# Optimization experiments

Measured on AMD Instinct MI355X. Metric: run time of the kernel, lower is better.

Reference implementation:

```python
import jax, jax.numpy as jnp
import numpy as np


def setup_inputs() -> dict:
    key = jax.random.key(0)
    k1, k2, k3, k4, k5 = jax.random.split(key, 5)
    H = W = 128
    C = 256
    N = 2000
    A = 7
    features_map = jax.random.normal(k1, (1, H, W, C), dtype=jnp.float32)
    # valid integer boxes: x2 > x1, y2 > y1, in-bounds
    x1 = jax.random.randint(k2, (N,), 0, W - 8)
    y1 = jax.random.randint(k3, (N,), 0, H - 8)
    bw = jax.random.randint(k4, (N,), 4, 48)
    bh = jax.random.randint(k5, (N,), 4, 48)
    x2 = jnp.minimum(x1 + bw, W)
    y2 = jnp.minimum(y1 + bh, H)
    boxes = jnp.stack([x1, y1, x2, y2], axis=-1).astype(jnp.int32)
    return {"features_map": features_map, "boxes": boxes, "anchor_size": A}


def reference(features_map, boxes, anchor_size):
    # Fused ROI pooling: per box, bilinear-resize the crop [y1:y2, x1:x2]
    # to (anchor_size, anchor_size), matching tf.image.resize bilinear
    # (half-pixel centers, edge clamped inside the crop).
    A = int(anchor_size)
    fm = features_map[0]  # [H, W, C]

    def axis_samples(lo, hi):
        span = (hi - lo).astype(jnp.float32)
        src = (jnp.arange(A, dtype=jnp.float32) + 0.5) * (span / A) - 0.5
        src = jnp.clip(src, 0.0, jnp.maximum(span - 1.0, 0.0))
        i0 = jnp.floor(src).astype(jnp.int32)
        i1 = jnp.minimum(i0 + 1, hi - lo - 1)
        frac = src - i0.astype(jnp.float32)
        return i0 + lo, i1 + lo, frac

    def pool_one(box):
        x1, y1, x2, y2 = box[0], box[1], box[2], box[3]
        ys0, ys1, fy = axis_samples(y1, y2)  # [A]
        xs0, xs1, fx = axis_samples(x1, x2)  # [A]
        v00 = fm[ys0[:, None], xs0[None, :]]  # [A, A, C]
        v01 = fm[ys0[:, None], xs1[None, :]]
        v10 = fm[ys1[:, None], xs0[None, :]]
        v11 = fm[ys1[:, None], xs1[None, :]]
        fy_ = fy[:, None, None]
        fx_ = fx[None, :, None]
        top = v00 * (1.0 - fx_) + v01 * fx_
        bot = v10 * (1.0 - fx_) + v11 * fx_
        return (top * (1.0 - fy_) + bot * fy_)[None]  # [1, A, A, C]

    return jax.vmap(pool_one)(boxes)  # [N, 1, A, A, C]
```

## Files before the change

kernel.cpp:

```cpp
#include <hip/hip_runtime.h>
#include <hip/hip_bf16.h>
#include <hip/hip_fp16.h>


#define FM_H 128
#define FM_W 128
#define FM_C 256
#define ANCH 7
#define NSAMP (ANCH * ANCH)
#define FM_ELEMS (FM_H * FM_W * FM_C)
#define CONV_BLOCKS 256

typedef float   f4 __attribute__((ext_vector_type(4)));
typedef _Float16 h4 __attribute__((ext_vector_type(4)));

__global__ __launch_bounds__(256) void prep_kernel(
    const float* __restrict__ fm, const int* __restrict__ boxes,
    _Float16* __restrict__ fm16, int* __restrict__ order,
    int n_boxes, int conv_blocks)
{
    if ((int)blockIdx.x < conv_blocks) {
        const int tid = blockIdx.x * 256 + threadIdx.x;
        const f4* src = (const f4*)fm;
        h4* dst = (h4*)fm16;
        #pragma unroll
        for (int k = 0; k < 16; ++k) {
            const int i = tid + k * 65536;
            const f4 v = src[i];
            h4 h;
            h[0] = (_Float16)v[0]; h[1] = (_Float16)v[1];
            h[2] = (_Float16)v[2]; h[3] = (_Float16)v[3];
            dst[i] = h;
        }
        return;
    }

    __shared__ int cursor[64];
    const int tid = threadIdx.x;
    if (tid < 64) cursor[tid] = 0;
    __syncthreads();

    for (int i = tid; i < n_boxes; i += 256) {
        const int x1 = boxes[i * 4 + 0];
        const int y1 = boxes[i * 4 + 1];
        const int key = ((y1 >> 4) << 3) | (x1 >> 4);
        atomicAdd(&cursor[key], 1);
    }
    __syncthreads();

    if (tid == 0) {
        int run = 0;
        for (int k = 0; k < 64; ++k) { int c = cursor[k]; cursor[k] = run; run += c; }
    }
    __syncthreads();

    for (int i = tid; i < n_boxes; i += 256) {
        const int x1 = boxes[i * 4 + 0];
        const int y1 = boxes[i * 4 + 1];
        const int key = ((y1 >> 4) << 3) | (x1 >> 4);
        const int pos = atomicAdd(&cursor[key], 1);
        order[pos] = i;
    }
}

template <typename ET, typename V4>
__global__ __launch_bounds__(256) void roi_pool_kernel_t(
    const ET* __restrict__ fmx,
    const int* __restrict__ boxes,
    const int* __restrict__ order,
    float* __restrict__ out,
    int n_samples)
{
    const int nb  = gridDim.x;
    const int b   = blockIdx.x;
    const int q   = nb >> 3;
    const int r   = nb & 7;
    const int xcd = b & 7;
    const int idx = b >> 3;
    const int sb  = (xcd < r ? xcd * (q + 1) : r * (q + 1) + (xcd - r) * q) + idx;

    const int lane = threadIdx.x & 63;
    const int wave = __builtin_amdgcn_readfirstlane((sb << 2) + (threadIdx.x >> 6));
    if (wave >= n_samples) return;

    const int sorted_box = wave / NSAMP;
    const int s   = wave - sorted_box * NSAMP;
    const int py  = s / ANCH;
    const int px  = s - py * ANCH;
    const int box = order ? order[sorted_box] : sorted_box;

    const int x1 = boxes[box * 4 + 0];
    const int y1 = boxes[box * 4 + 1];
    const int x2 = boxes[box * 4 + 2];
    const int y2 = boxes[box * 4 + 3];

    const float spany = (float)(y2 - y1);
    float sy = ((float)py + 0.5f) * (spany / (float)ANCH) - 0.5f;
    sy = fminf(fmaxf(sy, 0.0f), fmaxf(spany - 1.0f, 0.0f));
    const int iy0 = (int)floorf(sy);
    const int iy1 = min(iy0 + 1, y2 - y1 - 1);
    const float fy = sy - (float)iy0;
    const int ys0 = iy0 + y1;
    const int ys1 = iy1 + y1;

    const float spanx = (float)(x2 - x1);
    float sx = ((float)px + 0.5f) * (spanx / (float)ANCH) - 0.5f;
    sx = fminf(fmaxf(sx, 0.0f), fmaxf(spanx - 1.0f, 0.0f));
    const int ix0 = (int)floorf(sx);
    const int ix1 = min(ix0 + 1, x2 - x1 - 1);
    const float fx = sx - (float)ix0;
    const int xs0 = ix0 + x1;
    const int xs1 = ix1 + x1;

    const V4* p00 = (const V4*)(fmx + ((size_t)(ys0 * FM_W + xs0)) * FM_C);
    const V4* p01 = (const V4*)(fmx + ((size_t)(ys0 * FM_W + xs1)) * FM_C);
    const V4* p10 = (const V4*)(fmx + ((size_t)(ys1 * FM_W + xs0)) * FM_C);
    const V4* p11 = (const V4*)(fmx + ((size_t)(ys1 * FM_W + xs1)) * FM_C);

    const V4 v00 = p00[lane];
    const V4 v01 = p01[lane];
    const V4 v10 = p10[lane];
    const V4 v11 = p11[lane];

    const float gx = 1.0f - fx;
    const float gy = 1.0f - fy;

    f4 res;
    #pragma unroll
    for (int c = 0; c < 4; ++c) {
        const float top = (float)v00[c] * gx + (float)v01[c] * fx;
        const float bot = (float)v10[c] * gx + (float)v11[c] * fx;
        res[c] = top * gy + bot * fy;
    }

    f4* dst = (f4*)(out + ((size_t)(box * NSAMP + s)) * FM_C);
    __builtin_nontemporal_store(res, &dst[lane]);
}

extern "C" void kernel_launch(void* const* d_in, const int* in_sizes, int n_in,
                              void* d_out, int out_size, void* d_ws, size_t ws_size,
                              hipStream_t stream) {
    const float* fm    = (const float*)d_in[0];
    const int*   boxes = (const int*)d_in[1];

    const int N = in_sizes[1] / 4;
    const int n_samples = N * NSAMP;
    float* out = (float*)d_out;

    const size_t f16_bytes   = (size_t)FM_ELEMS * sizeof(_Float16);
    const size_t order_bytes = (size_t)N * sizeof(int);

    const int threads = 256;
    const int grid = (n_samples + 3) / 4;

    if (ws_size >= f16_bytes + order_bytes) {
        _Float16* fm16 = (_Float16*)d_ws;
        int* order = (int*)((char*)d_ws + f16_bytes);

        prep_kernel<<<CONV_BLOCKS + 1, 256, 0, stream>>>(
            fm, boxes, fm16, order, N, CONV_BLOCKS);
        roi_pool_kernel_t<_Float16, h4><<<grid, threads, 0, stream>>>(
            fm16, boxes, order, out, n_samples);
    } else if (ws_size >= order_bytes) {
        int* order = (int*)d_ws;
        prep_kernel<<<1, 256, 0, stream>>>(fm, boxes, nullptr, order, N, 0);
        roi_pool_kernel_t<float, f4><<<grid, threads, 0, stream>>>(
            fm, boxes, order, out, n_samples);
    } else {
        roi_pool_kernel_t<float, f4><<<grid, threads, 0, stream>>>(
            fm, boxes, nullptr, out, n_samples);
    }
}
```

Measured before the change: 34.98 us.

## Load adjacent pixel pair as one contiguous row segment and exchange halves via shuffle

```diff
diff --git a/kernel.cpp b/kernel.cpp
--- a/kernel.cpp
+++ b/kernel.cpp
@@ -7,12 +7,13 @@
 #define FM_W 128
 #define FM_C 256
 #define ANCH 7
-#define NSAMP (ANCH * ANCH)
+#define NSAMP 49
 #define FM_ELEMS (FM_H * FM_W * FM_C)
 #define CONV_BLOCKS 256
 
-typedef float   f4 __attribute__((ext_vector_type(4)));
-typedef _Float16 h4 __attribute__((ext_vector_type(4)));
+typedef float    f4 __attribute__((ext_vector_type(4)));
+typedef _Float16 h8 __attribute__((ext_vector_type(8)));
+typedef int      i4 __attribute__((ext_vector_type(4)));
 
 __global__ __launch_bounds__(256) void prep_kernel(
     const float* __restrict__ fm, const int* __restrict__ boxes,
@@ -22,12 +23,13 @@
     if ((int)blockIdx.x < conv_blocks) {
         const int tid = blockIdx.x * 256 + threadIdx.x;
         const f4* src = (const f4*)fm;
-        h4* dst = (h4*)fm16;
+        typedef _Float16 h4v __attribute__((ext_vector_type(4)));
+        h4v* dst = (h4v*)fm16;
         #pragma unroll
         for (int k = 0; k < 16; ++k) {
             const int i = tid + k * 65536;
             const f4 v = src[i];
-            h4 h;
+            h4v h;
             h[0] = (_Float16)v[0]; h[1] = (_Float16)v[1];
             h[2] = (_Float16)v[2]; h[3] = (_Float16)v[3];
             dst[i] = h;
@@ -63,9 +65,8 @@
     }
 }
 
-template <typename ET, typename V4>
-__global__ __launch_bounds__(256) void roi_pool_kernel_t(
-    const ET* __restrict__ fmx,
+__global__ __launch_bounds__(256) void roi_pair_kernel(
+    const _Float16* __restrict__ fm16,
     const int* __restrict__ boxes,
     const int* __restrict__ order,
     float* __restrict__ out,
@@ -87,7 +88,7 @@
     const int s   = wave - sorted_box * NSAMP;
     const int py  = s / ANCH;
     const int px  = s - py * ANCH;
-    const int box = order ? order[sorted_box] : sorted_box;
+    const int box = order[sorted_box];
 
     const int x1 = boxes[box * 4 + 0];
     const int y1 = boxes[box * 4 + 1];
@@ -95,7 +96,7 @@
     const int y2 = boxes[box * 4 + 3];
 
     const float spany = (float)(y2 - y1);
-    float sy = ((float)py + 0.5f) * (spany / (float)ANCH) - 0.5f;
+    float sy = ((float)py + 0.5f) * (spany / 7.0f) - 0.5f;
     sy = fminf(fmaxf(sy, 0.0f), fmaxf(spany - 1.0f, 0.0f));
     const int iy0 = (int)floorf(sy);
     const int iy1 = min(iy0 + 1, y2 - y1 - 1);
@@ -104,7 +105,7 @@
     const int ys1 = iy1 + y1;
 
     const float spanx = (float)(x2 - x1);
-    float sx = ((float)px + 0.5f) * (spanx / (float)ANCH) - 0.5f;
+    float sx = ((float)px + 0.5f) * (spanx / 7.0f) - 0.5f;
     sx = fminf(fmaxf(sx, 0.0f), fmaxf(spanx - 1.0f, 0.0f));
     const int ix0 = (int)floorf(sx);
     const int ix1 = min(ix0 + 1, x2 - x1 - 1);
@@ -112,28 +113,92 @@
     const int xs0 = ix0 + x1;
     const int xs1 = ix1 + x1;
 
-    const V4* p00 = (const V4*)(fmx + ((size_t)(ys0 * FM_W + xs0)) * FM_C);
-    const V4* p01 = (const V4*)(fmx + ((size_t)(ys0 * FM_W + xs1)) * FM_C);
-    const V4* p10 = (const V4*)(fmx + ((size_t)(ys1 * FM_W + xs0)) * FM_C);
-    const V4* p11 = (const V4*)(fmx + ((size_t)(ys1 * FM_W + xs1)) * FM_C);
-
-    const V4 v00 = p00[lane];
-    const V4 v01 = p01[lane];
-    const V4 v10 = p10[lane];
-    const V4 v11 = p11[lane];
+    const int p  = min(xs0, FM_W - 2);
+    const int h0 = xs0 - p;
+    const int h1 = xs1 - p;
+    const int H  = lane >> 5;
+
+    const h8* r0 = (const h8*)(fm16 + ((size_t)(ys0 * FM_W + p)) * FM_C);
+    const h8* r1 = (const h8*)(fm16 + ((size_t)(ys1 * FM_W + p)) * FM_C);
+    const h8 own0 = r0[lane];
+    const h8 own1 = r1[lane];
+
+    i4 o0 = __builtin_bit_cast(i4, own0);
+    i4 o1 = __builtin_bit_cast(i4, own1);
+    i4 s0v, s1v;
+    #pragma unroll
+    for (int k = 0; k < 4; ++k) {
+        s0v[k] = __shfl_xor(o0[k], 32, 64);
+        s1v[k] = __shfl_xor(o1[k], 32, 64);
+    }
+    const h8 shf0 = __builtin_bit_cast(h8, s0v);
+    const h8 shf1 = __builtin_bit_cast(h8, s1v);
+
+    const h8 v00 = (h0 == H) ? own0 : shf0;
+    const h8 v01 = (h1 == H) ? own0 : shf0;
+    const h8 v10 = (h0 == H) ? own1 : shf1;
+    const h8 v11 = (h1 == H) ? own1 : shf1;
 
     const float gx = 1.0f - fx;
     const float gy = 1.0f - fy;
 
-    f4 res;
-    #pragma unroll
-    for (int c = 0; c < 4; ++c) {
+    float res[8];
+    #pragma unroll
+    for (int c = 0; c < 8; ++c) {
         const float top = (float)v00[c] * gx + (float)v01[c] * fx;
         const float bot = (float)v10[c] * gx + (float)v11[c] * fx;
         res[c] = top * gy + bot * fy;
     }
 
-    f4* dst = (f4*)(out + ((size_t)(box * NSAMP + s)) * FM_C);
+    f4 sv;
+    #pragma unroll
+    for (int k = 0; k < 4; ++k) sv[k] = H ? res[4 + k] : res[k];
+
+    float* dst = out + ((size_t)(box * NSAMP + s)) * FM_C + (lane & 31) * 8 + H * 4;
+    __builtin_nontemporal_store(sv, (f4*)dst);
+}
+
+__global__ __launch_bounds__(256) void roi_gather_kernel(
+    const float* __restrict__ fm, const int* __restrict__ boxes,
+    float* __restrict__ out, int n_samples)
+{
+    const int lane = threadIdx.x & 63;
+    const int wave = (blockIdx.x << 2) + (threadIdx.x >> 6);
+    if (wave >= n_samples) return;
+    const int box = wave / NSAMP;
+    const int s   = wave - box * NSAMP;
+    const int py  = s / ANCH;
+    const int px  = s - py * ANCH;
+    const int x1 = boxes[box*4+0], y1 = boxes[box*4+1];
+    const int x2 = boxes[box*4+2], y2 = boxes[box*4+3];
+    const float spany = (float)(y2 - y1);
+    float sy = ((float)py + 0.5f) * (spany / 7.0f) - 0.5f;
+    sy = fminf(fmaxf(sy, 0.0f), fmaxf(spany - 1.0f, 0.0f));
+    const int iy0 = (int)floorf(sy);
+    const int iy1 = min(iy0 + 1, y2 - y1 - 1);
+    const float fy = sy - (float)iy0;
+    const int ys0 = iy0 + y1, ys1 = iy1 + y1;
+    const float spanx = (float)(x2 - x1);
+    float sx = ((float)px + 0.5f) * (spanx / 7.0f) - 0.5f;
+    sx = fminf(fmaxf(sx, 0.0f), fmaxf(spanx - 1.0f, 0.0f));
+    const int ix0 = (int)floorf(sx);
+    const int ix1 = min(ix0 + 1, x2 - x1 - 1);
+    const float fx = sx - (float)ix0;
+    const int xs0 = ix0 + x1, xs1 = ix1 + x1;
+    const f4* p00 = (const f4*)(fm + ((size_t)(ys0*FM_W+xs0))*FM_C);
+    const f4* p01 = (const f4*)(fm + ((size_t)(ys0*FM_W+xs1))*FM_C);
+    const f4* p10 = (const f4*)(fm + ((size_t)(ys1*FM_W+xs0))*FM_C);
+    const f4* p11 = (const f4*)(fm + ((size_t)(ys1*FM_W+xs1))*FM_C);
+    const f4 v00 = p00[lane], v01 = p01[lane], v10 = p10[lane], v11 = p11[lane];
+    const float gx = 1.0f - fx, gy = 1.0f - fy;
+    f4 res;
+    #pragma unroll
+    for (int c = 0; c < 4; ++c) {
+        const float top = v00[c] * gx + v01[c] * fx;
+        const float bot = v10[c] * gx + v11[c] * fx;
+        res[c] = top * gy + bot * fy;
+    }
+    f4* dst = (f4*)(out + (size_t)wave * FM_C);
     __builtin_nontemporal_store(res, &dst[lane]);
 }
 
@@ -159,15 +224,10 @@
 
         prep_kernel<<<CONV_BLOCKS + 1, 256, 0, stream>>>(
             fm, boxes, fm16, order, N, CONV_BLOCKS);
-        roi_pool_kernel_t<_Float16, h4><<<grid, threads, 0, stream>>>(
+        roi_pair_kernel<<<grid, threads, 0, stream>>>(
             fm16, boxes, order, out, n_samples);
-    } else if (ws_size >= order_bytes) {
-        int* order = (int*)d_ws;
-        prep_kernel<<<1, 256, 0, stream>>>(fm, boxes, nullptr, order, N, 0);
-        roi_pool_kernel_t<float, f4><<<grid, threads, 0, stream>>>(
-            fm, boxes, order, out, n_samples);
     } else {
-        roi_pool_kernel_t<float, f4><<<grid, threads, 0, stream>>>(
-            fm, boxes, nullptr, out, n_samples);
-    }
-}
+        roi_gather_kernel<<<grid, threads, 0, stream>>>(
+            fm, boxes, out, n_samples);
+    }
+}
```

After: 65.89 us. 1.88x slower.
